# Optimization experiments

Hardware: AMD Instinct MI355X
Metric: run time of the kernel (lower is better)

## Reference

```python
import jax, jax.numpy as jnp
import numpy as np

WIRES = 12
NQ = WIRES // 3          # 4 qubits per register
NF = 2 ** NQ             # 16 features per register
NW = 2 * NQ              # 8 wires in StronglyEntanglingLayers
NL = 1                   # n_layers
B = 2048
C64 = jnp.complex64

# constant gate matrices
H2 = jnp.asarray(np.array([[1.0, 1.0], [1.0, -1.0]]) / np.sqrt(2.0), C64)
CZ4 = jnp.asarray(np.diag([1.0, 1.0, 1.0, -1.0]), C64)
_cn = np.eye(4); _cn[2, 2] = _cn[3, 3] = 0.0; _cn[2, 3] = _cn[3, 2] = 1.0
CNOT4 = jnp.asarray(_cn, C64)
_tf = np.eye(8); _tf[6, 6] = _tf[7, 7] = 0.0; _tf[6, 7] = _tf[7, 6] = 1.0
TOF8 = jnp.asarray(_tf, C64)


def apply_gate(psi, U, wires):
    """Apply a k-qubit gate U (2^k x 2^k) to batched statevector psi: (B, 2,...,2)."""
    k = len(wires)
    axes = [w + 1 for w in wires]  # axis 0 is batch
    Ut = U.reshape((2,) * (2 * k))
    psi = jnp.tensordot(Ut, psi, axes=(list(range(k, 2 * k)), axes))
    return jnp.moveaxis(psi, list(range(k)), axes)


def rot_matrix(phi, theta, omega):
    """PennyLane Rot(phi, theta, omega) = RZ(omega) RY(theta) RZ(phi)."""
    c = jnp.cos(theta * 0.5).astype(C64)
    s = jnp.sin(theta * 0.5).astype(C64)
    ep = jnp.exp(-0.5j * (phi + omega).astype(C64))
    em = jnp.exp(0.5j * (phi - omega).astype(C64))
    return jnp.stack([jnp.stack([ep * c, -em * s]),
                      jnp.stack([jnp.conj(em) * s, jnp.conj(ep) * c])])


def _forward(x, weights):
    b = x.shape[0]
    # Mottonen state prep on wires 0-3 (f1) and 4-7 (f2); ancillas 8-11 start in |0>
    outer = x[:, :NF, None] * x[:, None, NF:]                     # (B, 16, 16)
    anc = jnp.zeros((2,) * NQ, jnp.float32).at[(0,) * NQ].set(1.0)
    psi = (outer.reshape((b,) + (2,) * (2 * NQ))[..., None, None, None, None] * anc).astype(C64)
    # StronglyEntanglingLayers: 1 layer, Rot per wire then range-1 CZ ring on wires 0..7
    for l in range(NL):
        for i in range(NW):
            psi = apply_gate(psi, rot_matrix(weights[l, i, 0], weights[l, i, 1], weights[l, i, 2]), [i])
        for i in range(NW):
            psi = apply_gate(psi, CZ4, [i, (i + 1) % NW])
    # measurement circuit: q1=0..3, q2=4..7, q3=8..11
    for i in range(NQ):
        psi = apply_gate(psi, CNOT4, [i, NQ + i])
        psi = apply_gate(psi, H2, [2 * NQ + i])
    for i in range(NQ):
        psi = apply_gate(psi, TOF8, [NQ + i, 2 * NQ + i, i])
    for i in range(NQ):
        psi = apply_gate(psi, CNOT4, [i, NQ + i])
        psi = apply_gate(psi, H2, [2 * NQ + i])
    # probs over wires 8..11, take element [0] (all ancillas |0>)
    psi0 = psi[..., 0, 0, 0, 0]                                   # (B, 2,...,2) over wires 0..7
    return jnp.sum(psi0.real ** 2 + psi0.imag ** 2, axis=tuple(range(1, 1 + 2 * NQ)))


def setup_inputs() -> dict:
    key = jax.random.key(0)
    k1, k2 = jax.random.split(key)
    x = jax.random.uniform(k1, (B, 2 * NF), jnp.float32, 0.05, 1.0)
    f1 = x[:, :NF] / jnp.linalg.norm(x[:, :NF], axis=1, keepdims=True)
    f2 = x[:, NF:] / jnp.linalg.norm(x[:, NF:], axis=1, keepdims=True)
    x = jnp.concatenate([f1, f2], axis=1)
    weights = jax.random.uniform(k2, (NL, NW, 3), jnp.float32, 0.0, 2.0 * np.pi)
    return {"x": x, "weights": weights}


def reference(x, weights):
    return _forward(x, weights)
```

## Files before the change

### kernel.cpp

```cpp
#include <hip/hip_runtime.h>


__global__ __launch_bounds__(256) void qattn_kernel(const float* __restrict__ x,
                                                    const float* __restrict__ w,
                                                    float* __restrict__ out) {
    const int b   = blockIdx.x;
    const int tid = threadIdx.x;

    __shared__ float sr[256];
    __shared__ float si[256];
    __shared__ float umat[8][8];
    __shared__ float wsum[4];

    if (tid < 8) {
        const float phi = w[tid * 3 + 0];
        const float th  = w[tid * 3 + 1];
        const float om  = w[tid * 3 + 2];
        float sh, ch;      sincosf(0.5f * th, &sh, &ch);
        float ep_i, ep_r;  sincosf(-0.5f * (phi + om), &ep_i, &ep_r);
        float em_i, em_r;  sincosf( 0.5f * (phi - om), &em_i, &em_r);
        umat[tid][0] =  ep_r * ch;
        umat[tid][1] =  ep_i * ch;
        umat[tid][2] = -em_r * sh;
        umat[tid][3] = -em_i * sh;
        umat[tid][4] =  em_r * sh;
        umat[tid][5] = -em_i * sh;
        umat[tid][6] =  ep_r * ch;
        umat[tid][7] = -ep_i * ch;
    }

    const float* xb = x + b * 32;
    float ar = xb[tid >> 4] * xb[16 + (tid & 15)];
    float ai = 0.0f;

    for (int g = 0; g < 8; ++g) {
        sr[tid] = ar; si[tid] = ai;
        __syncthreads();
        const int   mask = 1 << (7 - g);
        const float pr = sr[tid ^ mask];
        const float pi = si[tid ^ mask];
        const float u0r = umat[g][0], u0i = umat[g][1];
        const float u1r = umat[g][2], u1i = umat[g][3];
        const float u2r = umat[g][4], u2i = umat[g][5];
        const float u3r = umat[g][6], u3i = umat[g][7];
        float nr, ni;
        if ((tid & mask) == 0) {
            nr = u0r * ar - u0i * ai + u1r * pr - u1i * pi;
            ni = u0r * ai + u0i * ar + u1r * pi + u1i * pr;
        } else {
            nr = u2r * pr - u2i * pi + u3r * ar - u3i * ai;
            ni = u2r * pi + u2i * pr + u3r * ai + u3i * ar;
        }
        ar = nr; ai = ni;
        __syncthreads();
    }

    {
        const unsigned t = (unsigned)tid;
        const unsigned u = ((t >> 1) | (t << 7)) & 0xffu;
        if (__popc(t & u) & 1) { ar = -ar; ai = -ai; }
    }

    const int masks[4] = {0x88, 0x44, 0x22, 0x11};
#pragma unroll
    for (int p = 0; p < 4; ++p) {
        sr[tid] = ar; si[tid] = ai;
        __syncthreads();
        const int m = masks[p];
        const int t = tid & m;
        if (t != 0 && t != m) {
            ar = 0.5f * (ar + sr[tid ^ m]);
            ai = 0.5f * (ai + si[tid ^ m]);
        }
        __syncthreads();
    }

    float val = ar * ar + ai * ai;
#pragma unroll
    for (int off = 32; off > 0; off >>= 1) val += __shfl_down(val, off, 64);
    if ((tid & 63) == 0) wsum[tid >> 6] = val;
    __syncthreads();
    if (tid == 0) out[b] = wsum[0] + wsum[1] + wsum[2] + wsum[3];
}

extern "C" void kernel_launch(void* const* d_in, const int* in_sizes, int n_in,
                              void* d_out, int out_size, void* d_ws, size_t ws_size,
                              hipStream_t stream) {
    const float* x   = (const float*)d_in[0];
    const float* w   = (const float*)d_in[1];
    float*       out = (float*)d_out;
    qattn_kernel<<<out_size, 256, 0, stream>>>(x, w, out);
}
```

Before: 11.40 us.

## Map one statevector per wavefront with register-held amplitudes and shuffle gates

Each 64-lane wavefront now holds one sample's 256 amplitudes, four per lane. Gates on qubits 0 and 4 are applied within a lane's registers and the rest through cross-lane xor shuffles. This removes the shared-memory round trips and block-wide barriers between gates, and packs four samples per block. The grid shrinks by four, so correctness relies on the batch size being a multiple of four, and the index remapping for the CZ parity and ancilla averaging has to be right.

```diff
diff --git a/kernel.cpp b/kernel.cpp
--- a/kernel.cpp
+++ b/kernel.cpp
@@ -4,13 +4,11 @@
 __global__ __launch_bounds__(256) void qattn_kernel(const float* __restrict__ x,
                                                     const float* __restrict__ w,
                                                     float* __restrict__ out) {
-    const int b   = blockIdx.x;
-    const int tid = threadIdx.x;
+    const int tid  = threadIdx.x;
+    const int lane = tid & 63;
+    const int b    = (blockIdx.x << 2) | (tid >> 6);
 
-    __shared__ float sr[256];
-    __shared__ float si[256];
     __shared__ float umat[8][8];
-    __shared__ float wsum[4];
 
     if (tid < 8) {
         const float phi = w[tid * 3 + 0];
@@ -30,57 +28,95 @@
     }
 
     const float* xb = x + b * 32;
-    float ar = xb[tid >> 4] * xb[16 + (tid & 15)];
-    float ai = 0.0f;
+    const int lh = lane >> 3, ll = lane & 7;
+    const float f1a = xb[lh],      f1b = xb[8 + lh];
+    const float f2a = xb[16 + ll], f2b = xb[24 + ll];
 
-    for (int g = 0; g < 8; ++g) {
-        sr[tid] = ar; si[tid] = ai;
-        __syncthreads();
-        const int   mask = 1 << (7 - g);
-        const float pr = sr[tid ^ mask];
-        const float pi = si[tid ^ mask];
-        const float u0r = umat[g][0], u0i = umat[g][1];
-        const float u1r = umat[g][2], u1i = umat[g][3];
-        const float u2r = umat[g][4], u2i = umat[g][5];
-        const float u3r = umat[g][6], u3i = umat[g][7];
-        float nr, ni;
-        if ((tid & mask) == 0) {
-            nr = u0r * ar - u0i * ai + u1r * pr - u1i * pi;
-            ni = u0r * ai + u0i * ar + u1r * pi + u1i * pr;
-        } else {
-            nr = u2r * pr - u2i * pi + u3r * ar - u3i * ai;
-            ni = u2r * pi + u2i * pr + u3r * ai + u3i * ar;
+    float ar[4] = { f1a * f2a, f1a * f2b, f1b * f2a, f1b * f2b };
+    float ai[4] = { 0.f, 0.f, 0.f, 0.f };
+
+    __syncthreads();
+
+    const int gw[6] = {1, 2, 3, 5, 6, 7};
+    const int gl[6] = {32, 16, 8, 4, 2, 1};
+#pragma unroll
+    for (int i = 0; i < 6; ++i) {
+        const int g = gw[i], L = gl[i];
+        const bool hi = (lane & L) != 0;
+        const float uar = hi ? umat[g][6] : umat[g][0];
+        const float uai = hi ? umat[g][7] : umat[g][1];
+        const float ubr = hi ? umat[g][4] : umat[g][2];
+        const float ubi = hi ? umat[g][5] : umat[g][3];
+#pragma unroll
+        for (int r = 0; r < 4; ++r) {
+            const float pr = __shfl_xor(ar[r], L, 64);
+            const float pi = __shfl_xor(ai[r], L, 64);
+            const float nr = uar * ar[r] - uai * ai[r] + ubr * pr - ubi * pi;
+            const float ni = uar * ai[r] + uai * ar[r] + ubr * pi + ubi * pr;
+            ar[r] = nr; ai[r] = ni;
         }
-        ar = nr; ai = ni;
-        __syncthreads();
     }
 
     {
-        const unsigned t = (unsigned)tid;
-        const unsigned u = ((t >> 1) | (t << 7)) & 0xffu;
-        if (__popc(t & u) & 1) { ar = -ar; ai = -ai; }
+        const float u0r=umat[0][0],u0i=umat[0][1],u1r=umat[0][2],u1i=umat[0][3];
+        const float u2r=umat[0][4],u2i=umat[0][5],u3r=umat[0][6],u3i=umat[0][7];
+#pragma unroll
+        for (int lo = 0; lo < 2; ++lo) {
+            const int h2 = lo + 2;
+            const float a0r=ar[lo],a0i=ai[lo],a1r=ar[h2],a1i=ai[h2];
+            ar[lo] = u0r*a0r-u0i*a0i + u1r*a1r-u1i*a1i;
+            ai[lo] = u0r*a0i+u0i*a0r + u1r*a1i+u1i*a1r;
+            ar[h2] = u2r*a0r-u2i*a0i + u3r*a1r-u3i*a1i;
+            ai[h2] = u2r*a0i+u2i*a0r + u3r*a1i+u3i*a1r;
+        }
+    }
+    {
+        const float u0r=umat[4][0],u0i=umat[4][1],u1r=umat[4][2],u1i=umat[4][3];
+        const float u2r=umat[4][4],u2i=umat[4][5],u3r=umat[4][6],u3i=umat[4][7];
+#pragma unroll
+        for (int p = 0; p < 2; ++p) {
+            const int lo = p * 2, h2 = lo + 1;
+            const float a0r=ar[lo],a0i=ai[lo],a1r=ar[h2],a1i=ai[h2];
+            ar[lo] = u0r*a0r-u0i*a0i + u1r*a1r-u1i*a1i;
+            ai[lo] = u0r*a0i+u0i*a0r + u1r*a1i+u1i*a1r;
+            ar[h2] = u2r*a0r-u2i*a0i + u3r*a1r-u3i*a1i;
+            ai[h2] = u2r*a0i+u2i*a0r + u3r*a1i+u3i*a1r;
+        }
     }
 
-    const int masks[4] = {0x88, 0x44, 0x22, 0x11};
 #pragma unroll
-    for (int p = 0; p < 4; ++p) {
-        sr[tid] = ar; si[tid] = ai;
-        __syncthreads();
-        const int m = masks[p];
-        const int t = tid & m;
-        if (t != 0 && t != m) {
-            ar = 0.5f * (ar + sr[tid ^ m]);
-            ai = 0.5f * (ai + si[tid ^ m]);
-        }
-        __syncthreads();
+    for (int r = 0; r < 4; ++r) {
+        const unsigned a = ((unsigned)(r & 2) << 6) | ((unsigned)(lane & 56) << 1)
+                         | ((unsigned)(r & 1) << 3) | (unsigned)(lane & 7);
+        const unsigned u = ((a >> 1) | (a << 7)) & 0xffu;
+        if (__popc(a & u) & 1) { ar[r] = -ar[r]; ai[r] = -ai[r]; }
     }
 
-    float val = ar * ar + ai * ai;
+    {
+        const float nr = 0.5f * (ar[1] + ar[2]);
+        const float ni = 0.5f * (ai[1] + ai[2]);
+        ar[1] = ar[2] = nr;  ai[1] = ai[2] = ni;
+    }
+    const int pm[3] = {36, 18, 9};
 #pragma unroll
-    for (int off = 32; off > 0; off >>= 1) val += __shfl_down(val, off, 64);
-    if ((tid & 63) == 0) wsum[tid >> 6] = val;
-    __syncthreads();
-    if (tid == 0) out[b] = wsum[0] + wsum[1] + wsum[2] + wsum[3];
+    for (int i = 0; i < 3; ++i) {
+        const int L = pm[i];
+        const bool diff = __popc(lane & L) & 1;
+#pragma unroll
+        for (int r = 0; r < 4; ++r) {
+            const float pr = __shfl_xor(ar[r], L, 64);
+            const float pi = __shfl_xor(ai[r], L, 64);
+            ar[r] = diff ? 0.5f * (ar[r] + pr) : ar[r];
+            ai[r] = diff ? 0.5f * (ai[r] + pi) : ai[r];
+        }
+    }
+
+    float val = 0.f;
+#pragma unroll
+    for (int r = 0; r < 4; ++r) val += ar[r] * ar[r] + ai[r] * ai[r];
+#pragma unroll
+    for (int off = 32; off; off >>= 1) val += __shfl_xor(val, off, 64);
+    if ((tid & 63) == 0) out[b] = val;
 }
 
 extern "C" void kernel_launch(void* const* d_in, const int* in_sizes, int n_in,
@@ -89,5 +125,5 @@
     const float* x   = (const float*)d_in[0];
     const float* w   = (const float*)d_in[1];
     float*       out = (float*)d_out;
-    qattn_kernel<<<out_size, 256, 0, stream>>>(x, w, out);
+    qattn_kernel<<<out_size / 4, 256, 0, stream>>>(x, w, out);
 }
```

After: 9.666 us. 15.2% less time.
